# Performance work log

Hardware: AMD Instinct MI355X
Metric: run time of the kernel (lower is better)

Reference implementation:

```python
import jax, jax.numpy as jnp
import numpy as np

N = 50000
E = 800000
D = 128


def setup_inputs() -> dict:
    key = jax.random.key(0)
    ks = jax.random.split(key, 6)
    x = jax.random.normal(ks[0], (N, D), dtype=jnp.float32)
    W_self = jax.random.normal(ks[1], (D, D), dtype=jnp.float32) * (1.0 / np.sqrt(D))
    b_self = jax.random.normal(ks[2], (D,), dtype=jnp.float32) * 0.01
    W_neigh = jax.random.normal(ks[3], (D, D), dtype=jnp.float32) * (1.0 / np.sqrt(D))
    src = jax.random.randint(ks[4], (E,), 0, N, dtype=jnp.int32)
    dst = jax.random.randint(ks[5], (E,), 0, N, dtype=jnp.int32)
    # Row-normalized adjacency: weight of edge (src -> dst) is 1/deg(dst)
    deg = jax.ops.segment_sum(jnp.ones((E,), jnp.float32), dst, num_segments=N)
    edge_w = 1.0 / jnp.maximum(deg, 1.0)[dst]
    return {"x": x, "W_self": W_self, "b_self": b_self, "W_neigh": W_neigh,
            "edge_w": edge_w, "src": src, "dst": dst}


def reference(x, W_self, b_self, W_neigh, edge_w, src, dst):
    n = x.shape[0]
    # neigh = A @ x  (row-normalized sparse adjacency as weighted edge list)
    msgs = x[src] * edge_w[:, None]               # (E, D) gather + scale
    neigh = jax.ops.segment_sum(msgs, dst, num_segments=n)  # (N, D) scatter-add
    # lin_self(x) + lin_neigh(neigh)  (torch Linear: y = x @ W.T + b)
    return x @ W_self.T + b_self + neigh @ W_neigh.T
```

## Files before the change

### kernel.cpp

```cpp
#include <hip/hip_runtime.h>
#include <hip/hip_bf16.h>

#define N_NODES 50000
#define N_EDGES 800000
#define DIM 128

#define RSH 6
#define RNODES 64
#define NRANGE 782
#define CH 4096
#define NB 196
#define NTOT (NRANGE * NB)
#define NSCANB ((NTOT + 1023) / 1024)
#define BCAP 64

typedef __attribute__((ext_vector_type(8))) short bf16x8;
typedef __attribute__((ext_vector_type(4))) float f32x4;

union BU8 { uint4 u; bf16x8 b; };

static __device__ __forceinline__ ushort f2bf(float f) {
    __hip_bfloat16 h = __float2bfloat16(f);
    return *reinterpret_cast<ushort*>(&h);
}
static __device__ __forceinline__ uint pack2(float a, float b) {
    return (uint)f2bf(a) | ((uint)f2bf(b) << 16);
}
static __device__ __forceinline__ float bflo(uint u) { return __uint_as_float(u << 16); }
static __device__ __forceinline__ float bfhi(uint u) { return __uint_as_float(u & 0xffff0000u); }

__global__ void cvtW_k(const float* __restrict__ Ws, const float* __restrict__ Wn,
                       ushort* __restrict__ Wcat, int* __restrict__ ovfcnt) {
    int t = blockIdx.x * blockDim.x + threadIdx.x;
    if (t == 0) *ovfcnt = 0;
    const float* srcp = (t < 2048) ? Ws : Wn;
    int i = (t & 2047) * 8;
    float4 a = *(const float4*)(srcp + i);
    float4 b = *(const float4*)(srcp + i + 4);
    uint4 r;
    r.x = pack2(a.x, a.y); r.y = pack2(a.z, a.w);
    r.z = pack2(b.x, b.y); r.w = pack2(b.z, b.w);
    *(uint4*)(Wcat + ((t < 2048) ? 0 : 16384) + i) = r;
}

__global__ __launch_bounds__(256) void hist_k(const int* __restrict__ dst,
                                              int* __restrict__ histg) {
    __shared__ int h[NRANGE];
    int t = threadIdx.x, b = blockIdx.x;
    for (int i = t; i < NRANGE; i += 256) h[i] = 0;
    __syncthreads();
    int e0 = b * CH;
    int n = N_EDGES - e0; if (n > CH) n = CH;
    for (int i = t; i < n; i += 256) atomicAdd(&h[dst[e0 + i] >> RSH], 1);
    __syncthreads();
    for (int i = t; i < NRANGE; i += 256) histg[b * NRANGE + i] = h[i];
}

__global__ __launch_bounds__(1024) void scanA_k(const int* __restrict__ histg,
                                                int* __restrict__ off,
                                                int* __restrict__ bsum) {
    __shared__ int lds[1024];
    int t = threadIdx.x;
    int c = blockIdx.x * 1024 + t;
    int v = 0;
    if (c < NTOT) {
        int r = c / NB, b = c - r * NB;
        v = histg[b * NRANGE + r];
    }
    lds[t] = v;
    __syncthreads();
    for (int s = 1; s < 1024; s <<= 1) {
        int add = (t >= s) ? lds[t - s] : 0;
        __syncthreads();
        lds[t] += add;
        __syncthreads();
    }
    if (c < NTOT) off[c] = lds[t] - v;
    if (t == 1023) bsum[blockIdx.x] = lds[1023];
}

__global__ __launch_bounds__(256) void scatter_k(const int* __restrict__ src,
                                                 const int* __restrict__ dst,
                                                 const int* __restrict__ off,
                                                 const int* __restrict__ bsum,
                                                 uint* __restrict__ buf) {
    __shared__ int cur[NRANGE];
    __shared__ int sb[256];
    int t = threadIdx.x, b = blockIdx.x;

    int v = (t < NSCANB) ? bsum[t] : 0;
    sb[t] = v;
    __syncthreads();
    for (int s = 1; s < 256; s <<= 1) {
        int add = (t >= s) ? sb[t - s] : 0;
        __syncthreads();
        sb[t] += add;
        __syncthreads();
    }
    sb[t] -= v;
    __syncthreads();

    for (int i = t; i < NRANGE; i += 256) {
        int c = i * NB + b;
        cur[i] = off[c] + sb[c >> 10];
    }
    __syncthreads();

    int e0 = b * CH;
    int n = N_EDGES - e0; if (n > CH) n = CH;
    for (int i = t; i < n; i += 256) {
        int e = e0 + i;
        int d = dst[e];
        int r = d >> RSH;
        int pos = atomicAdd(&cur[r], 1);
        buf[pos] = ((uint)src[e] << RSH) | (uint)(d & (RNODES - 1));
    }
}

__global__ __launch_bounds__(256, 2) void mm_k(const float* __restrict__ x,
                                               const ushort* __restrict__ Wcat,
                                               const float* __restrict__ bias,
                                               float* __restrict__ out,
                                               ushort* __restrict__ Yn) {
    __shared__ ushort wlds[32768];
    int tid  = threadIdx.x;
    int lane = tid & 63;
    int w    = tid >> 6;
    int lr   = lane & 15;
    int g    = lane >> 4;
    int myrow0 = blockIdx.x * 128 + w * 32;

    bf16x8 a[2][4];
#pragma unroll
    for (int rt = 0; rt < 2; ++rt) {
        int row = myrow0 + rt * 16 + lr;
        bool ok = row < N_NODES;
        const float* ap = x + (size_t)row * 128;
#pragma unroll
        for (int kf = 0; kf < 4; ++kf) {
            float4 f0 = make_float4(0.f, 0.f, 0.f, 0.f), f1 = f0;
            if (ok) {
                f0 = *(const float4*)(ap + kf * 32 + g * 8);
                f1 = *(const float4*)(ap + kf * 32 + g * 8 + 4);
            }
            BU8 u;
            u.u.x = pack2(f0.x, f0.y); u.u.y = pack2(f0.z, f0.w);
            u.u.z = pack2(f1.x, f1.y); u.u.w = pack2(f1.z, f1.w);
            a[rt][kf] = u.b;
        }
    }

#pragma unroll
    for (int i = 0; i < 16; ++i) {
        int f = i * 256 + tid;
        int r = f >> 4, c = f & 15;
        uint4 v = *(const uint4*)(Wcat + r * 128 + c * 8);
        *(uint4*)(&wlds[r * 128 + ((c ^ (r & 7)) * 8)]) = v;
    }
    __syncthreads();

    f32x4 acc[2][16];
#pragma unroll
    for (int rt = 0; rt < 2; ++rt)
#pragma unroll
        for (int nt = 0; nt < 16; ++nt) acc[rt][nt] = (f32x4){0.f, 0.f, 0.f, 0.f};

#pragma unroll
    for (int nt = 0; nt < 16; ++nt) {
        int row = nt * 16 + lr;
#pragma unroll
        for (int kf = 0; kf < 4; ++kf) {
            int chunk = kf * 4 + g;
            bf16x8 b = *(const bf16x8*)(&wlds[row * 128 + ((chunk ^ (lr & 7)) * 8)]);
            acc[0][nt] = __builtin_amdgcn_mfma_f32_16x16x32_bf16(a[0][kf], b, acc[0][nt], 0, 0, 0);
            acc[1][nt] = __builtin_amdgcn_mfma_f32_16x16x32_bf16(a[1][kf], b, acc[1][nt], 0, 0, 0);
        }
    }

#pragma unroll
    for (int nt = 0; nt < 16; ++nt) {
        int col = nt * 16 + lr;
        float bv = (col < 128) ? bias[col] : 0.f;
#pragma unroll
        for (int rt = 0; rt < 2; ++rt) {
            int rowb = myrow0 + rt * 16 + g * 4;
#pragma unroll
            for (int j = 0; j < 4; ++j) {
                int row = rowb + j;
                if (row < N_NODES) {
                    if (col < 128)
                        out[(size_t)row * 128 + col] = acc[rt][nt][j] + bv;
                    else
                        Yn[(size_t)row * 128 + (col - 128)] = f2bf(acc[rt][nt][j]);
                }
            }
        }
    }
}

__global__ __launch_bounds__(512) void agg4_k(const ushort* __restrict__ Yn,
                                              const uint* __restrict__ buf,
                                              const int* __restrict__ off,
                                              const int* __restrict__ bsum,
                                              float* __restrict__ out,
                                              int* __restrict__ count,
                                              int* __restrict__ ovfcnt,
                                              int2* __restrict__ ovf) {
    __shared__ ushort bkt[RNODES][BCAP];
    __shared__ int cnt[RNODES];
    __shared__ int sb[256];
    int r = blockIdx.x;
    int t = threadIdx.x;
    if (t < RNODES) cnt[t] = 0;

    int v = 0;
    if (t < 256) {
        v = (t < NSCANB) ? bsum[t] : 0;
        sb[t] = v;
    }
    __syncthreads();
    for (int s = 1; s < 256; s <<= 1) {
        int add = 0;
        if (t < 256 && t >= s) add = sb[t - s];
        __syncthreads();
        if (t < 256) sb[t] += add;
        __syncthreads();
    }
    if (t < 256) sb[t] -= v;
    __syncthreads();

    int c0 = r * NB;
    int start = off[c0] + sb[c0 >> 10];
    int end;
    if (r == NRANGE - 1) end = N_EDGES;
    else { int c1 = (r + 1) * NB; end = off[c1] + sb[c1 >> 10]; }

    for (int i = start + t; i < end; i += 512) {
        uint p = buf[i];
        int local = (int)(p & (RNODES - 1));
        int s = (int)(p >> RSH);
        int pos = atomicAdd(&cnt[local], 1);
        if (pos < BCAP) {
            bkt[local][pos] = (ushort)s;
        } else {
            int o = atomicAdd(ovfcnt, 1);
            ovf[o] = make_int2(s, r * RNODES + local);
        }
    }
    __syncthreads();

    int lane = t & 63;
    int wv = t >> 6;
    int g = lane >> 4;
    int c8 = (lane & 15) * 8;

#pragma unroll 1
    for (int q = 0; q < 8; ++q) {
        int n = wv * 8 + q;
        int gnode = r * RNODES + n;
        if (gnode >= N_NODES) continue;
        int deg = cnt[n];
        if (lane == 0) count[gnode] = deg;
        int m = (deg < BCAP) ? deg : BCAP;
        int sreg = (lane < m) ? (int)bkt[n][lane] : 0;

        float acc0 = 0.f, acc1 = 0.f, acc2 = 0.f, acc3 = 0.f;
        float acc4 = 0.f, acc5 = 0.f, acc6 = 0.f, acc7 = 0.f;

#define ACC8(v)                                        \
    do {                                               \
        acc0 += bflo(v.x); acc1 += bfhi(v.x);          \
        acc2 += bflo(v.y); acc3 += bfhi(v.y);          \
        acc4 += bflo(v.z); acc5 += bfhi(v.z);          \
        acc6 += bflo(v.w); acc7 += bfhi(v.w);          \
    } while (0)

        int j = 0;
        for (; j + 4 <= m; j += 4) {
            int s = __shfl(sreg, j + g);
            uint4 vv = *(const uint4*)(Yn + (size_t)s * 128 + c8);
            ACC8(vv);
        }
        if (j < m) {
            int jj = j + g;
            bool valid = jj < m;
            int s = __shfl(sreg, valid ? jj : j);
            uint4 vv = *(const uint4*)(Yn + (size_t)s * 128 + c8);
            if (valid) ACC8(vv);
        }
#undef ACC8

#define RED(a) do { a += __shfl_xor(a, 16); a += __shfl_xor(a, 32); } while (0)
        RED(acc0); RED(acc1); RED(acc2); RED(acc3);
        RED(acc4); RED(acc5); RED(acc6); RED(acc7);
#undef RED

        if (lane < 16) {
            float scale = 1.0f / (float)(deg > 0 ? deg : 1);
            float* orow = out + (size_t)gnode * 128 + c8;
            float4 o0 = *(const float4*)(orow);
            float4 o1 = *(const float4*)(orow + 4);
            o0.x += scale * acc0; o0.y += scale * acc1;
            o0.z += scale * acc2; o0.w += scale * acc3;
            o1.x += scale * acc4; o1.y += scale * acc5;
            o1.z += scale * acc6; o1.w += scale * acc7;
            *(float4*)(orow) = o0;
            *(float4*)(orow + 4) = o1;
        }
    }
}

__global__ void ovf_k(const ushort* __restrict__ Yn, const int* __restrict__ count,
                      const int* __restrict__ ovfcnt, const int2* __restrict__ ovf,
                      float* __restrict__ out) {
    int n = *ovfcnt;
    for (int i = blockIdx.x; i < n; i += gridDim.x) {
        int2 e = ovf[i];
        int s = e.x, d = e.y;
        float scale = 1.0f / (float)max(count[d], 1);
        int c = threadIdx.x;
        float v = __uint_as_float(((uint)Yn[(size_t)s * 128 + c]) << 16);
        atomicAdd(&out[(size_t)d * 128 + c], scale * v);
    }
}

extern "C" void kernel_launch(void* const* d_in, const int* in_sizes, int n_in,
                              void* d_out, int out_size, void* d_ws, size_t ws_size,
                              hipStream_t stream) {
    const float* x       = (const float*)d_in[0];
    const float* W_self  = (const float*)d_in[1];
    const float* b_self  = (const float*)d_in[2];
    const float* W_neigh = (const float*)d_in[3];
    const int* src = (const int*)d_in[5];
    const int* dst = (const int*)d_in[6];
    float* out = (float*)d_out;

    char* ws = (char*)d_ws;
    ushort* Yn     = (ushort*)(ws);
    ushort* Wcat   = (ushort*)(ws + 12800000);
    int*    histg  = (int*)(ws + 12865536);
    int*    off    = (int*)(ws + 13478624);
    uint*   buf    = (uint*)(ws + 14091712);
    int*    count  = (int*)(ws + 17291712);
    int*    ovfcnt = (int*)(ws + 17491712);
    int*    bsum   = (int*)(ws + 17491728);
    int2*   ovf    = (int2*)(ws + 17492752);

    cvtW_k<<<16, 256, 0, stream>>>(W_self, W_neigh, Wcat, ovfcnt);
    mm_k<<<(N_NODES + 127) / 128, 256, 0, stream>>>(x, Wcat, b_self, out, Yn);

    hist_k<<<NB, 256, 0, stream>>>(dst, histg);
    scanA_k<<<NSCANB, 1024, 0, stream>>>(histg, off, bsum);
    scatter_k<<<NB, 256, 0, stream>>>(src, dst, off, bsum, buf);

    agg4_k<<<NRANGE, 512, 0, stream>>>(Yn, buf, off, bsum, out, count, ovfcnt, ovf);

    ovf_k<<<64, 128, 0, stream>>>(Yn, count, ovfcnt, ovf, out);
}
```

Measured before the change: 90.62 us.

## Fuse weight conversion and dst histogram into the matmul kernel launch

Removes the separate cvtW and hist kernels. Each matmul block now converts fp32 weights to bf16 on the fly while staging them into LDS, and extra blocks appended to the same grid compute the per-range dst histogram in reused shared memory. This cuts two kernel launches and the serialization between them, and lets the histogram run alongside the GEMM. The cost is that every matmul block reads 128KB of fp32 weights instead of 64KB of bf16 and does redundant conversion work.

```diff
diff --git a/kernel.cpp b/kernel.cpp
--- a/kernel.cpp
+++ b/kernel.cpp
@@ -13,6 +13,7 @@
 #define NTOT (NRANGE * NB)
 #define NSCANB ((NTOT + 1023) / 1024)
 #define BCAP 64
+#define MM_BLOCKS ((N_NODES + 127) / 128)
 
 typedef __attribute__((ext_vector_type(8))) short bf16x8;
 typedef __attribute__((ext_vector_type(4))) float f32x4;
@@ -29,31 +30,110 @@
 static __device__ __forceinline__ float bflo(uint u) { return __uint_as_float(u << 16); }
 static __device__ __forceinline__ float bfhi(uint u) { return __uint_as_float(u & 0xffff0000u); }
 
-__global__ void cvtW_k(const float* __restrict__ Ws, const float* __restrict__ Wn,
-                       ushort* __restrict__ Wcat, int* __restrict__ ovfcnt) {
-    int t = blockIdx.x * blockDim.x + threadIdx.x;
-    if (t == 0) *ovfcnt = 0;
-    const float* srcp = (t < 2048) ? Ws : Wn;
-    int i = (t & 2047) * 8;
-    float4 a = *(const float4*)(srcp + i);
-    float4 b = *(const float4*)(srcp + i + 4);
-    uint4 r;
-    r.x = pack2(a.x, a.y); r.y = pack2(a.z, a.w);
-    r.z = pack2(b.x, b.y); r.w = pack2(b.z, b.w);
-    *(uint4*)(Wcat + ((t < 2048) ? 0 : 16384) + i) = r;
-}
-
-__global__ __launch_bounds__(256) void hist_k(const int* __restrict__ dst,
-                                              int* __restrict__ histg) {
-    __shared__ int h[NRANGE];
-    int t = threadIdx.x, b = blockIdx.x;
-    for (int i = t; i < NRANGE; i += 256) h[i] = 0;
-    __syncthreads();
-    int e0 = b * CH;
-    int n = N_EDGES - e0; if (n > CH) n = CH;
-    for (int i = t; i < n; i += 256) atomicAdd(&h[dst[e0 + i] >> RSH], 1);
-    __syncthreads();
-    for (int i = t; i < NRANGE; i += 256) histg[b * NRANGE + i] = h[i];
+__global__ __launch_bounds__(256, 2) void mmhist_k(const float* __restrict__ x,
+                                                   const float* __restrict__ Ws,
+                                                   const float* __restrict__ Wn,
+                                                   const float* __restrict__ bias,
+                                                   const int* __restrict__ dst,
+                                                   float* __restrict__ out,
+                                                   ushort* __restrict__ Yn,
+                                                   int* __restrict__ histg,
+                                                   int* __restrict__ ovfcnt) {
+    __shared__ ushort wlds[32768];
+    int tid = threadIdx.x;
+
+    if (blockIdx.x >= MM_BLOCKS) {
+        int b = blockIdx.x - MM_BLOCKS;
+        if (b == 0 && tid == 0) *ovfcnt = 0;
+        int* h = (int*)wlds;
+        for (int i = tid; i < NRANGE; i += 256) h[i] = 0;
+        __syncthreads();
+        int e0 = b * CH;
+        int n = N_EDGES - e0; if (n > CH) n = CH;
+        for (int i = tid; i < n; i += 256) atomicAdd(&h[dst[e0 + i] >> RSH], 1);
+        __syncthreads();
+        for (int i = tid; i < NRANGE; i += 256) histg[b * NRANGE + i] = h[i];
+        return;
+    }
+
+    int lane = tid & 63;
+    int w    = tid >> 6;
+    int lr   = lane & 15;
+    int g    = lane >> 4;
+    int myrow0 = blockIdx.x * 128 + w * 32;
+
+    bf16x8 a[2][4];
+#pragma unroll
+    for (int rt = 0; rt < 2; ++rt) {
+        int row = myrow0 + rt * 16 + lr;
+        bool ok = row < N_NODES;
+        const float* ap = x + (size_t)row * 128;
+#pragma unroll
+        for (int kf = 0; kf < 4; ++kf) {
+            float4 f0 = make_float4(0.f, 0.f, 0.f, 0.f), f1 = f0;
+            if (ok) {
+                f0 = *(const float4*)(ap + kf * 32 + g * 8);
+                f1 = *(const float4*)(ap + kf * 32 + g * 8 + 4);
+            }
+            BU8 u;
+            u.u.x = pack2(f0.x, f0.y); u.u.y = pack2(f0.z, f0.w);
+            u.u.z = pack2(f1.x, f1.y); u.u.w = pack2(f1.z, f1.w);
+            a[rt][kf] = u.b;
+        }
+    }
+
+#pragma unroll
+    for (int i = 0; i < 16; ++i) {
+        int f = i * 256 + tid;
+        int r = f >> 4, c = f & 15;
+        const float* wsrc = ((r < 128) ? (Ws + (size_t)r * 128)
+                                       : (Wn + (size_t)(r - 128) * 128)) + c * 8;
+        float4 f0 = *(const float4*)(wsrc);
+        float4 f1 = *(const float4*)(wsrc + 4);
+        uint4 u;
+        u.x = pack2(f0.x, f0.y); u.y = pack2(f0.z, f0.w);
+        u.z = pack2(f1.x, f1.y); u.w = pack2(f1.z, f1.w);
+        *(uint4*)(&wlds[r * 128 + ((c ^ (r & 7)) * 8)]) = u;
+    }
+    __syncthreads();
+
+    f32x4 acc[2][16];
+#pragma unroll
+    for (int rt = 0; rt < 2; ++rt)
+#pragma unroll
+        for (int nt = 0; nt < 16; ++nt) acc[rt][nt] = (f32x4){0.f, 0.f, 0.f, 0.f};
+
+#pragma unroll
+    for (int nt = 0; nt < 16; ++nt) {
+        int row = nt * 16 + lr;
+#pragma unroll
+        for (int kf = 0; kf < 4; ++kf) {
+            int chunk = kf * 4 + g;
+            bf16x8 b = *(const bf16x8*)(&wlds[row * 128 + ((chunk ^ (lr & 7)) * 8)]);
+            acc[0][nt] = __builtin_amdgcn_mfma_f32_16x16x32_bf16(a[0][kf], b, acc[0][nt], 0, 0, 0);
+            acc[1][nt] = __builtin_amdgcn_mfma_f32_16x16x32_bf16(a[1][kf], b, acc[1][nt], 0, 0, 0);
+        }
+    }
+
+#pragma unroll
+    for (int nt = 0; nt < 16; ++nt) {
+        int col = nt * 16 + lr;
+        float bv = (col < 128) ? bias[col] : 0.f;
+#pragma unroll
+        for (int rt = 0; rt < 2; ++rt) {
+            int rowb = myrow0 + rt * 16 + g * 4;
+#pragma unroll
+            for (int j = 0; j < 4; ++j) {
+                int row = rowb + j;
+                if (row < N_NODES) {
+                    if (col < 128)
+                        out[(size_t)row * 128 + col] = acc[rt][nt][j] + bv;
+                    else
+                        Yn[(size_t)row * 128 + (col - 128)] = f2bf(acc[rt][nt][j]);
+                }
+            }
+        }
+    }
 }
 
 __global__ __launch_bounds__(1024) void scanA_k(const int* __restrict__ histg,
@@ -114,87 +194,6 @@
         int r = d >> RSH;
         int pos = atomicAdd(&cur[r], 1);
         buf[pos] = ((uint)src[e] << RSH) | (uint)(d & (RNODES - 1));
-    }
-}
-
-__global__ __launch_bounds__(256, 2) void mm_k(const float* __restrict__ x,
-                                               const ushort* __restrict__ Wcat,
-                                               const float* __restrict__ bias,
-                                               float* __restrict__ out,
-                                               ushort* __restrict__ Yn) {
-    __shared__ ushort wlds[32768];
-    int tid  = threadIdx.x;
-    int lane = tid & 63;
-    int w    = tid >> 6;
-    int lr   = lane & 15;
-    int g    = lane >> 4;
-    int myrow0 = blockIdx.x * 128 + w * 32;
-
-    bf16x8 a[2][4];
-#pragma unroll
-    for (int rt = 0; rt < 2; ++rt) {
-        int row = myrow0 + rt * 16 + lr;
-        bool ok = row < N_NODES;
-        const float* ap = x + (size_t)row * 128;
-#pragma unroll
-        for (int kf = 0; kf < 4; ++kf) {
-            float4 f0 = make_float4(0.f, 0.f, 0.f, 0.f), f1 = f0;
-            if (ok) {
-                f0 = *(const float4*)(ap + kf * 32 + g * 8);
-                f1 = *(const float4*)(ap + kf * 32 + g * 8 + 4);
-            }
-            BU8 u;
-            u.u.x = pack2(f0.x, f0.y); u.u.y = pack2(f0.z, f0.w);
-            u.u.z = pack2(f1.x, f1.y); u.u.w = pack2(f1.z, f1.w);
-            a[rt][kf] = u.b;
-        }
-    }
-
-#pragma unroll
-    for (int i = 0; i < 16; ++i) {
-        int f = i * 256 + tid;
-        int r = f >> 4, c = f & 15;
-        uint4 v = *(const uint4*)(Wcat + r * 128 + c * 8);
-        *(uint4*)(&wlds[r * 128 + ((c ^ (r & 7)) * 8)]) = v;
-    }
-    __syncthreads();
-
-    f32x4 acc[2][16];
-#pragma unroll
-    for (int rt = 0; rt < 2; ++rt)
-#pragma unroll
-        for (int nt = 0; nt < 16; ++nt) acc[rt][nt] = (f32x4){0.f, 0.f, 0.f, 0.f};
-
-#pragma unroll
-    for (int nt = 0; nt < 16; ++nt) {
-        int row = nt * 16 + lr;
-#pragma unroll
-        for (int kf = 0; kf < 4; ++kf) {
-            int chunk = kf * 4 + g;
-            bf16x8 b = *(const bf16x8*)(&wlds[row * 128 + ((chunk ^ (lr & 7)) * 8)]);
-            acc[0][nt] = __builtin_amdgcn_mfma_f32_16x16x32_bf16(a[0][kf], b, acc[0][nt], 0, 0, 0);
-            acc[1][nt] = __builtin_amdgcn_mfma_f32_16x16x32_bf16(a[1][kf], b, acc[1][nt], 0, 0, 0);
-        }
-    }
-
-#pragma unroll
-    for (int nt = 0; nt < 16; ++nt) {
-        int col = nt * 16 + lr;
-        float bv = (col < 128) ? bias[col] : 0.f;
-#pragma unroll
-        for (int rt = 0; rt < 2; ++rt) {
-            int rowb = myrow0 + rt * 16 + g * 4;
-#pragma unroll
-            for (int j = 0; j < 4; ++j) {
-                int row = rowb + j;
-                if (row < N_NODES) {
-                    if (col < 128)
-                        out[(size_t)row * 128 + col] = acc[rt][nt][j] + bv;
-                    else
-                        Yn[(size_t)row * 128 + (col - 128)] = f2bf(acc[rt][nt][j]);
-                }
-            }
-        }
     }
 }
 
@@ -337,19 +336,17 @@
 
     char* ws = (char*)d_ws;
     ushort* Yn     = (ushort*)(ws);
-    ushort* Wcat   = (ushort*)(ws + 12800000);
-    int*    histg  = (int*)(ws + 12865536);
-    int*    off    = (int*)(ws + 13478624);
-    uint*   buf    = (uint*)(ws + 14091712);
-    int*    count  = (int*)(ws + 17291712);
-    int*    ovfcnt = (int*)(ws + 17491712);
-    int*    bsum   = (int*)(ws + 17491728);
-    int2*   ovf    = (int2*)(ws + 17492752);
-
-    cvtW_k<<<16, 256, 0, stream>>>(W_self, W_neigh, Wcat, ovfcnt);
-    mm_k<<<(N_NODES + 127) / 128, 256, 0, stream>>>(x, Wcat, b_self, out, Yn);
-
-    hist_k<<<NB, 256, 0, stream>>>(dst, histg);
+    int*    histg  = (int*)(ws + 12800000);
+    int*    off    = (int*)(ws + 13413088);
+    uint*   buf    = (uint*)(ws + 14026176);
+    int*    count  = (int*)(ws + 17226176);
+    int*    ovfcnt = (int*)(ws + 17426176);
+    int*    bsum   = (int*)(ws + 17426192);
+    int2*   ovf    = (int2*)(ws + 17427216);
+
+    mmhist_k<<<MM_BLOCKS + NB, 256, 0, stream>>>(x, W_self, W_neigh, b_self, dst,
+                                                 out, Yn, histg, ovfcnt);
+
     scanA_k<<<NSCANB, 1024, 0, stream>>>(histg, off, bsum);
     scatter_k<<<NB, 256, 0, stream>>>(src, dst, off, bsum, buf);
 
```

After: 84.80 us. -6.4%, faster.
